# Optimization experiments

Hardware: AMD Instinct MI355X
Metric: run time of the kernel (lower is better)

The kernel has to match this reference:

```python
import jax, jax.numpy as jnp
import numpy as np

N_NODES = 50000
D_FEAT = 128
N_EDGES_1 = 800_000
N_EDGES_2 = 2_400_000


def setup_inputs() -> dict:
    key = jax.random.key(0)
    k = jax.random.split(key, 7)
    x = jax.random.normal(k[0], (N_NODES, D_FEAT), dtype=jnp.float32)
    row1 = jax.random.randint(k[1], (N_EDGES_1,), 0, N_NODES, dtype=jnp.int32)
    col1 = jax.random.randint(k[2], (N_EDGES_1,), 0, N_NODES, dtype=jnp.int32)
    vals1 = jax.random.uniform(k[3], (N_EDGES_1,), dtype=jnp.float32)
    row2 = jax.random.randint(k[4], (N_EDGES_2,), 0, N_NODES, dtype=jnp.int32)
    col2 = jax.random.randint(k[5], (N_EDGES_2,), 0, N_NODES, dtype=jnp.int32)
    vals2 = jax.random.uniform(k[6], (N_EDGES_2,), dtype=jnp.float32)
    return {"x": x, "row1": row1, "col1": col1, "vals1": vals1,
            "row2": row2, "col2": col2, "vals2": vals2}


def _spmm(row, col, vals, x, n_nodes):
    # (A @ x)[i] = sum_{e: row[e]==i} vals[e] * x[col[e]]
    msgs = vals[:, None] * x[col]          # [E, d] gathered, weighted messages
    return jax.ops.segment_sum(msgs, row, num_segments=n_nodes)  # [N, d]


def reference(x, row1, col1, vals1, row2, col2, vals2):
    x1 = _spmm(row1, col1, vals1, x, N_NODES)   # 1-hop aggregation
    x2 = _spmm(row2, col2, vals2, x, N_NODES)   # 2-hop aggregation
    return jnp.concatenate([x1, x2], axis=1)    # [N, 2d]
```

## Files before the change

kernel.cpp:

```cpp
#include <hip/hip_runtime.h>


constexpr int D = 128;
constexpr int OUT_STRIDE = 256;
constexpr int NBMAX = 800;
constexpr int BATCH = 4096;
constexpr int LRECS = 3840;

struct KP {
  const float* x;
  const int* row1; const int* col1; const float* vals1;
  const int* row2; const int* col2; const float* vals2;
  float* out;
  int n, e1, e2, nx4, nb, cap1, cap2, t1, ntasks;
  int* gcur;
  int* counts;
  int* base;
  unsigned short* xb;
  uint2* seg1;
  uint2* seg2;
};

__device__ __forceinline__ unsigned short f2b(float f) {
  unsigned u = __float_as_uint(f);
  u += 0x7fffu + ((u >> 16) & 1u);
  return (unsigned short)(u >> 16);
}
__device__ __forceinline__ float blo(unsigned u) { return __uint_as_float(u << 16); }
__device__ __forceinline__ float bhi(unsigned u) { return __uint_as_float(u & 0xffff0000u); }

__launch_bounds__(256)
__global__ void cvt_k(KP p) {
  const int i = blockIdx.x * 256 + threadIdx.x;
  const int GT = gridDim.x * 256;
  for (int j = i; j < p.nx4; j += GT) {
    const float4 v = ((const float4*)p.x)[j];
    ushort4 o; o.x = f2b(v.x); o.y = f2b(v.y); o.z = f2b(v.z); o.w = f2b(v.w);
    ((ushort4*)p.xb)[j] = o;
  }
}

__launch_bounds__(256)
__global__ void count_k(KP p) {
  __shared__ int cnts[NBMAX];
  const int tid = threadIdx.x;
  const int nb  = p.nb;
  const int task  = blockIdx.x;
  const int hop   = (task >= p.t1);
  const int tbase = (hop ? (task - p.t1) : task) * BATCH;
  const int E     = hop ? p.e2 : p.e1;
  const int m     = min(BATCH, E - tbase);
  const int* rowp = hop ? p.row2 : p.row1;

  for (int b = tid; b < NBMAX; b += 256) cnts[b] = 0;
  __syncthreads();

  #pragma unroll
  for (int k = 0; k < BATCH / 1024; ++k) {
    const int i4 = tid + k * 256;
    const int e0 = i4 * 4;
    if (e0 < m) {
      if (e0 + 3 < m) {
        const int4 r = ((const int4*)(rowp + tbase))[i4];
        atomicAdd(&cnts[r.x >> 6], 1);
        atomicAdd(&cnts[r.y >> 6], 1);
        atomicAdd(&cnts[r.z >> 6], 1);
        atomicAdd(&cnts[r.w >> 6], 1);
      } else {
        for (int j = e0; j < m; ++j) atomicAdd(&cnts[rowp[tbase + j] >> 6], 1);
      }
    }
  }
  __syncthreads();

  int* crow = p.counts + (size_t)task * nb;
  for (int b = tid; b < nb; b += 256) crow[b] = cnts[b];
}

__launch_bounds__(256)
__global__ void scan_k(KP p) {
  const int lane = threadIdx.x & 63;
  const int gb   = blockIdx.x * 4 + (threadIdx.x >> 6);
  const int nb   = p.nb;
  if (gb >= 2 * nb) return;
  const int hop = (gb >= nb);
  const int b   = hop ? gb - nb : gb;
  const int t0  = hop ? p.t1 : 0;
  const int te  = hop ? p.ntasks : p.t1;

  int carry = 0;
  for (int tc = t0; tc < te; tc += 64) {
    const int t = tc + lane;
    const int c = (t < te) ? p.counts[(size_t)t * nb + b] : 0;
    int acc = c;
    #pragma unroll
    for (int d = 1; d < 64; d <<= 1) { int u = __shfl_up(acc, d); if (lane >= d) acc += u; }
    if (t < te) p.base[(size_t)t * nb + b] = carry + acc - c;
    carry += __shfl(acc, 63);
  }
  if (lane == 0) p.gcur[hop * nb + b] = carry;
}

__launch_bounds__(256)
__global__ void scatter_k(KP p) {
  __shared__ uint2 srecs[BATCH];
  __shared__ int lstart[NBMAX];
  __shared__ int curs[NBMAX];
  __shared__ int gbase[NBMAX];
  __shared__ int wsum[4];
  const int tid  = threadIdx.x;
  const int lane = tid & 63;
  const int wid  = tid >> 6;
  const int nb   = p.nb;

  const int task  = blockIdx.x;
  const int hop   = (task >= p.t1);
  const int tbase = (hop ? (task - p.t1) : task) * BATCH;
  const int E     = hop ? p.e2 : p.e1;
  const int m     = min(BATCH, E - tbase);
  const int* rowp = hop ? p.row2 : p.row1;
  const int* colp = hop ? p.col2 : p.col1;
  const float* vp = hop ? p.vals2 : p.vals1;
  const int cap   = hop ? p.cap2 : p.cap1;
  uint2* seg      = hop ? p.seg2 : p.seg1;
  const int* brow = p.base   + (size_t)task * nb;
  const int* crow = p.counts + (size_t)task * nb;

  __shared__ int cnts[NBMAX];
  for (int b = tid; b < nb; b += 256) { gbase[b] = brow[b]; cnts[b] = crow[b]; }
  for (int b = nb + tid; b < NBMAX; b += 256) cnts[b] = 0;
  __syncthreads();

  int c0 = 0, c1 = 0, c2 = 0, c3 = 0, s = 0;
  const int b0 = tid * 4;
  if (b0 < NBMAX) {
    c0 = cnts[b0]; c1 = cnts[b0 + 1]; c2 = cnts[b0 + 2]; c3 = cnts[b0 + 3];
    s = c0 + c1 + c2 + c3;
  }
  int acc = s;
  #pragma unroll
  for (int d = 1; d < 64; d <<= 1) { int t = __shfl_up(acc, d); if (lane >= d) acc += t; }
  if (lane == 63) wsum[wid] = acc;
  __syncthreads();
  int woff = 0;
  #pragma unroll
  for (int w = 0; w < 4; ++w) if (w < wid) woff += wsum[w];
  if (b0 < NBMAX) {
    const int ex = woff + acc - s;
    lstart[b0]     = ex;                curs[b0]     = ex;
    lstart[b0 + 1] = ex + c0;           curs[b0 + 1] = ex + c0;
    lstart[b0 + 2] = ex + c0 + c1;      curs[b0 + 2] = ex + c0 + c1;
    lstart[b0 + 3] = ex + c0 + c1 + c2; curs[b0 + 3] = ex + c0 + c1 + c2;
  }
  __syncthreads();

  #pragma unroll
  for (int k = 0; k < BATCH / 1024; ++k) {
    const int i4 = tid + k * 256;
    const int e0 = i4 * 4;
    if (e0 < m) {
      if (e0 + 3 < m) {
        const int4  rr = ((const int4*)(rowp + tbase))[i4];
        const int4  cc = ((const int4*)(colp + tbase))[i4];
        const float4 vv = ((const float4*)(vp + tbase))[i4];
        {
          const int r = rr.x, b = r >> 6;
          const unsigned meta = (unsigned)cc.x | ((unsigned)(r & 63) << 16) | ((unsigned)b << 22);
          srecs[atomicAdd(&curs[b], 1)] = make_uint2(meta, __float_as_uint(vv.x));
        }
        {
          const int r = rr.y, b = r >> 6;
          const unsigned meta = (unsigned)cc.y | ((unsigned)(r & 63) << 16) | ((unsigned)b << 22);
          srecs[atomicAdd(&curs[b], 1)] = make_uint2(meta, __float_as_uint(vv.y));
        }
        {
          const int r = rr.z, b = r >> 6;
          const unsigned meta = (unsigned)cc.z | ((unsigned)(r & 63) << 16) | ((unsigned)b << 22);
          srecs[atomicAdd(&curs[b], 1)] = make_uint2(meta, __float_as_uint(vv.z));
        }
        {
          const int r = rr.w, b = r >> 6;
          const unsigned meta = (unsigned)cc.w | ((unsigned)(r & 63) << 16) | ((unsigned)b << 22);
          srecs[atomicAdd(&curs[b], 1)] = make_uint2(meta, __float_as_uint(vv.w));
        }
      } else {
        for (int j = e0; j < m; ++j) {
          const int r = rowp[tbase + j], b = r >> 6;
          const unsigned meta = (unsigned)colp[tbase + j] | ((unsigned)(r & 63) << 16) | ((unsigned)b << 22);
          srecs[atomicAdd(&curs[b], 1)] = make_uint2(meta, __float_as_uint(vp[tbase + j]));
        }
      }
    }
  }
  __syncthreads();

  for (int t = tid; t < m; t += 256) {
    const uint2 rec = srecs[t];
    const int b = rec.x >> 22;
    const int pos = gbase[b] + (t - lstart[b]);
    if (pos < cap) seg[(size_t)b * cap + pos] = rec;
  }
}

__launch_bounds__(256)
__global__ void sort_gather_k(KP p) {
  __shared__ uint2 lrecs[LRECS];
  __shared__ int rstart[65];
  __shared__ int lcur[64];
  const int tid  = threadIdx.x;
  const int lane = tid & 63;
  const int wid  = tid >> 6;
  const int nb   = p.nb;
  const int hop  = (blockIdx.x < nb) ? 1 : 0;
  const int b    = hop ? blockIdx.x : blockIdx.x - nb;
  const int cap  = hop ? p.cap2 : p.cap1;
  const uint2* seg = (hop ? p.seg2 : p.seg1) + (size_t)b * cap;
  const int cnt  = min(p.gcur[(hop ? nb : 0) + b], cap);
  const uint4* xq = (const uint4*)p.xb;

  if (tid < 64) lcur[tid] = 0;
  __syncthreads();
  for (int t = tid; t < cnt; t += 256)
    atomicAdd(&lcur[(seg[t].x >> 16) & 63u], 1);
  __syncthreads();

  if (tid < 64) {
    const int c = lcur[tid];
    int acc = c;
    #pragma unroll
    for (int d = 1; d < 64; d <<= 1) { int t = __shfl_up(acc, d); if (lane >= d) acc += t; }
    const int ex = acc - c;
    rstart[tid] = ex;
    lcur[tid] = ex;
    if (tid == 63) rstart[64] = acc;
  }
  __syncthreads();

  for (int t = tid; t < cnt; t += 256) {
    const uint2 rec = seg[t];
    const int rl = (int)((rec.x >> 16) & 63u);
    const int pos = atomicAdd(&lcur[rl], 1);
    lrecs[pos] = rec;
  }
  __syncthreads();

  const int g   = lane >> 4;
  const int sub = lane & 15;
  const int rbase = b * 64;

  for (int r = wid; r < 64; r += 4) {
    const int rg = rbase + r;
    if (rg >= p.n) break;
    const int rs = rstart[r];
    const int re = rstart[r + 1];
    float a0 = 0.f, a1 = 0.f, a2 = 0.f, a3 = 0.f;
    float a4 = 0.f, a5 = 0.f, a6 = 0.f, a7 = 0.f;
    if (re > rs) {
      auto LD = [&](int idx, float& v, uint4& xv) {
        const uint2 q = lrecs[idx < re ? idx : re - 1];
        v = (idx < re) ? __uint_as_float(q.y) : 0.f;
        xv = xq[(q.x & 0xffffu) * 16u + (unsigned)sub];
      };
      #define FMA_G(v, xv)                                            \
        a0 = fmaf(v, blo(xv.x), a0); a1 = fmaf(v, bhi(xv.x), a1);     \
        a2 = fmaf(v, blo(xv.y), a2); a3 = fmaf(v, bhi(xv.y), a3);     \
        a4 = fmaf(v, blo(xv.z), a4); a5 = fmaf(v, bhi(xv.z), a5);     \
        a6 = fmaf(v, blo(xv.w), a6); a7 = fmaf(v, bhi(xv.w), a7);

      float v0, v1, v2, v3; uint4 x0, x1, x2, x3;
      const int j0 = rs + g;
      LD(j0, v0, x0); LD(j0 + 4, v1, x1); LD(j0 + 8, v2, x2); LD(j0 + 12, v3, x3);
      const int iters = (re - rs + 15) >> 4;
      for (int it = 1; it < iters; ++it) {
        const int jn = j0 + (it << 4);
        FMA_G(v0, x0); LD(jn,      v0, x0);
        FMA_G(v1, x1); LD(jn + 4,  v1, x1);
        FMA_G(v2, x2); LD(jn + 8,  v2, x2);
        FMA_G(v3, x3); LD(jn + 12, v3, x3);
      }
      FMA_G(v0, x0); FMA_G(v1, x1); FMA_G(v2, x2); FMA_G(v3, x3);
      #undef FMA_G

      a0 += __shfl_xor(a0, 16); a0 += __shfl_xor(a0, 32);
      a1 += __shfl_xor(a1, 16); a1 += __shfl_xor(a1, 32);
      a2 += __shfl_xor(a2, 16); a2 += __shfl_xor(a2, 32);
      a3 += __shfl_xor(a3, 16); a3 += __shfl_xor(a3, 32);
      a4 += __shfl_xor(a4, 16); a4 += __shfl_xor(a4, 32);
      a5 += __shfl_xor(a5, 16); a5 += __shfl_xor(a5, 32);
      a6 += __shfl_xor(a6, 16); a6 += __shfl_xor(a6, 32);
      a7 += __shfl_xor(a7, 16); a7 += __shfl_xor(a7, 32);
    }
    if (g == 0) {
      float* op = p.out + (size_t)rg * OUT_STRIDE + hop * D + sub * 8;
      ((float4*)op)[0] = make_float4(a0, a1, a2, a3);
      ((float4*)op)[1] = make_float4(a4, a5, a6, a7);
    }
  }
}

extern "C" void kernel_launch(void* const* d_in, const int* in_sizes, int n_in,
                              void* d_out, int out_size, void* d_ws, size_t ws_size,
                              hipStream_t stream) {
  KP p;
  p.x     = (const float*)d_in[0];
  p.row1  = (const int*)  d_in[1];
  p.col1  = (const int*)  d_in[2];
  p.vals1 = (const float*)d_in[3];
  p.row2  = (const int*)  d_in[4];
  p.col2  = (const int*)  d_in[5];
  p.vals2 = (const float*)d_in[6];
  p.out   = (float*)d_out;

  p.e1  = in_sizes[1];
  p.e2  = in_sizes[4];
  p.n   = out_size / OUT_STRIDE;
  p.nx4 = in_sizes[0] / 4;
  p.nb  = (p.n + 63) >> 6;
  if (p.nb > NBMAX || p.n > 65535) return;

  {
    const float m1 = (float)p.e1 / p.nb, m2 = (float)p.e2 / p.nb;
    p.cap1 = ((int)(m1 + 10.f * __builtin_sqrtf(m1) + 64.f) + 7) & ~7;
    p.cap2 = ((int)(m2 + 10.f * __builtin_sqrtf(m2) + 64.f) + 7) & ~7;
    if (p.cap1 > LRECS) p.cap1 = LRECS;
    if (p.cap2 > LRECS) p.cap2 = LRECS;
  }
  p.t1     = (p.e1 + BATCH - 1) / BATCH;
  p.ntasks = p.t1 + (p.e2 + BATCH - 1) / BATCH;

  char* w = (char*)d_ws;
  size_t off = 0;
  p.gcur = (int*)w;                       off += (size_t)(2 * p.nb) * 4;
  off = (off + 15) & ~(size_t)15;
  p.xb   = (unsigned short*)(w + off);    off += (size_t)in_sizes[0] * 2;
  off = (off + 15) & ~(size_t)15;
  p.seg1 = (uint2*)(w + off);             off += (size_t)p.nb * p.cap1 * 8;
  p.seg2 = (uint2*)(w + off);             off += (size_t)p.nb * p.cap2 * 8;
  off = (off + 15) & ~(size_t)15;
  p.counts = (int*)(w + off);             off += (size_t)p.ntasks * p.nb * 4;
  off = (off + 15) & ~(size_t)15;
  p.base = (int*)(w + off);               off += (size_t)p.ntasks * p.nb * 4;
  if (ws_size < off) return;

  cvt_k     <<<1024,      256, 0, stream>>>(p);
  count_k   <<<p.ntasks,  256, 0, stream>>>(p);
  scan_k    <<<(2 * p.nb + 3) / 4, 256, 0, stream>>>(p);
  scatter_k <<<p.ntasks,  256, 0, stream>>>(p);
  sort_gather_k<<<2 * p.nb, 256, 0, stream>>>(p);
}
```

Before: 277.1 us.

## Split bf16 feature table into four column slabs and gather per slab

```diff
diff --git a/kernel.cpp b/kernel.cpp
--- a/kernel.cpp
+++ b/kernel.cpp
@@ -36,7 +36,11 @@
   for (int j = i; j < p.nx4; j += GT) {
     const float4 v = ((const float4*)p.x)[j];
     ushort4 o; o.x = f2b(v.x); o.y = f2b(v.y); o.z = f2b(v.z); o.w = f2b(v.w);
-    ((ushort4*)p.xb)[j] = o;
+    const int node = j >> 5;
+    const int f4   = j & 31;
+    const int q    = f4 >> 3;
+    const int k    = f4 & 7;
+    ((ushort4*)p.xb)[((size_t)q * p.n + node) * 8 + k] = o;
   }
 }
 
@@ -216,7 +220,6 @@
   const int cap  = hop ? p.cap2 : p.cap1;
   const uint2* seg = (hop ? p.seg2 : p.seg1) + (size_t)b * cap;
   const int cnt  = min(p.gcur[(hop ? nb : 0) + b], cap);
-  const uint4* xq = (const uint4*)p.xb;
 
   if (tid < 64) lcur[tid] = 0;
   __syncthreads();
@@ -244,57 +247,57 @@
   }
   __syncthreads();
 
-  const int g   = lane >> 4;
-  const int sub = lane & 15;
+  const int g   = lane >> 2;
+  const int sub = lane & 3;
   const int rbase = b * 64;
 
-  for (int r = wid; r < 64; r += 4) {
-    const int rg = rbase + r;
-    if (rg >= p.n) break;
-    const int rs = rstart[r];
-    const int re = rstart[r + 1];
-    float a0 = 0.f, a1 = 0.f, a2 = 0.f, a3 = 0.f;
-    float a4 = 0.f, a5 = 0.f, a6 = 0.f, a7 = 0.f;
-    if (re > rs) {
-      auto LD = [&](int idx, float& v, uint4& xv) {
-        const uint2 q = lrecs[idx < re ? idx : re - 1];
-        v = (idx < re) ? __uint_as_float(q.y) : 0.f;
-        xv = xq[(q.x & 0xffffu) * 16u + (unsigned)sub];
-      };
-      #define FMA_G(v, xv)                                            \
-        a0 = fmaf(v, blo(xv.x), a0); a1 = fmaf(v, bhi(xv.x), a1);     \
-        a2 = fmaf(v, blo(xv.y), a2); a3 = fmaf(v, bhi(xv.y), a3);     \
-        a4 = fmaf(v, blo(xv.z), a4); a5 = fmaf(v, bhi(xv.z), a5);     \
-        a6 = fmaf(v, blo(xv.w), a6); a7 = fmaf(v, bhi(xv.w), a7);
-
-      float v0, v1, v2, v3; uint4 x0, x1, x2, x3;
-      const int j0 = rs + g;
-      LD(j0, v0, x0); LD(j0 + 4, v1, x1); LD(j0 + 8, v2, x2); LD(j0 + 12, v3, x3);
-      const int iters = (re - rs + 15) >> 4;
-      for (int it = 1; it < iters; ++it) {
-        const int jn = j0 + (it << 4);
-        FMA_G(v0, x0); LD(jn,      v0, x0);
-        FMA_G(v1, x1); LD(jn + 4,  v1, x1);
-        FMA_G(v2, x2); LD(jn + 8,  v2, x2);
-        FMA_G(v3, x3); LD(jn + 12, v3, x3);
+  for (int q = 0; q < 4; ++q) {
+    const uint4* xq = (const uint4*)(p.xb + (size_t)q * p.n * 32);
+    for (int r = wid; r < 64; r += 4) {
+      const int rg = rbase + r;
+      if (rg >= p.n) break;
+      const int rs = rstart[r];
+      const int re = rstart[r + 1];
+      float a0 = 0.f, a1 = 0.f, a2 = 0.f, a3 = 0.f;
+      float a4 = 0.f, a5 = 0.f, a6 = 0.f, a7 = 0.f;
+      if (re > rs) {
+        auto LD = [&](int idx, float& v, uint4& xv) {
+          const uint2 rr = lrecs[idx < re ? idx : re - 1];
+          v = (idx < re) ? __uint_as_float(rr.y) : 0.f;
+          xv = xq[(size_t)(rr.x & 0xffffu) * 4u + (unsigned)sub];
+        };
+        #define FMA_G(v, xv)                                            \
+          a0 = fmaf(v, blo(xv.x), a0); a1 = fmaf(v, bhi(xv.x), a1);     \
+          a2 = fmaf(v, blo(xv.y), a2); a3 = fmaf(v, bhi(xv.y), a3);     \
+          a4 = fmaf(v, blo(xv.z), a4); a5 = fmaf(v, bhi(xv.z), a5);     \
+          a6 = fmaf(v, blo(xv.w), a6); a7 = fmaf(v, bhi(xv.w), a7);
+
+        float vA; uint4 xA;
+        LD(rs + g, vA, xA);
+        for (int jn = rs + 16; jn < re; jn += 16) {
+          float vB; uint4 xB;
+          LD(jn + g, vB, xB);
+          FMA_G(vA, xA);
+          vA = vB; xA = xB;
+        }
+        FMA_G(vA, xA);
+        #undef FMA_G
+
+        #pragma unroll
+        for (int d = 4; d < 64; d <<= 1) {
+          a0 += __shfl_xor(a0, d); a1 += __shfl_xor(a1, d);
+          a2 += __shfl_xor(a2, d); a3 += __shfl_xor(a3, d);
+          a4 += __shfl_xor(a4, d); a5 += __shfl_xor(a5, d);
+          a6 += __shfl_xor(a6, d); a7 += __shfl_xor(a7, d);
+        }
       }
-      FMA_G(v0, x0); FMA_G(v1, x1); FMA_G(v2, x2); FMA_G(v3, x3);
-      #undef FMA_G
-
-      a0 += __shfl_xor(a0, 16); a0 += __shfl_xor(a0, 32);
-      a1 += __shfl_xor(a1, 16); a1 += __shfl_xor(a1, 32);
-      a2 += __shfl_xor(a2, 16); a2 += __shfl_xor(a2, 32);
-      a3 += __shfl_xor(a3, 16); a3 += __shfl_xor(a3, 32);
-      a4 += __shfl_xor(a4, 16); a4 += __shfl_xor(a4, 32);
-      a5 += __shfl_xor(a5, 16); a5 += __shfl_xor(a5, 32);
-      a6 += __shfl_xor(a6, 16); a6 += __shfl_xor(a6, 32);
-      a7 += __shfl_xor(a7, 16); a7 += __shfl_xor(a7, 32);
+      if (g == 0) {
+        float* op = p.out + (size_t)rg * OUT_STRIDE + hop * D + q * 32 + sub * 8;
+        ((float4*)op)[0] = make_float4(a0, a1, a2, a3);
+        ((float4*)op)[1] = make_float4(a4, a5, a6, a7);
+      }
     }
-    if (g == 0) {
-      float* op = p.out + (size_t)rg * OUT_STRIDE + hop * D + sub * 8;
-      ((float4*)op)[0] = make_float4(a0, a1, a2, a3);
-      ((float4*)op)[1] = make_float4(a4, a5, a6, a7);
-    }
+    __syncthreads();
   }
 }
 
```

New measurement: 345.6 us. +24.7%, slower.
